# Optimization experiments

Measured on AMD Instinct MI355X. Metric: run time of the kernel, lower is better.

The kernel has to match this reference:

```python
import jax, jax.numpy as jnp
import numpy as np

ACT_MIN, ACT_MAX = -127.0, 127.0      # 8-bit symmetric
W_MIN, W_MAX = -127.0, 127.0          # 8-bit symmetric
B_MIN, B_MAX = -32767.0, 32767.0      # 16-bit symmetric
ALPHA = 10.0                          # clipped-ReLU ceiling


def fake_quant(x, min_v, max_v):
    # 'scale' quantization: per-tensor symmetric scale from max-abs,
    # round -> clamp -> dequant; straight-through estimator for grads.
    scale = max_v / jnp.max(jnp.abs(x))
    q = jnp.clip(jnp.round(x * scale), min_v, max_v) / scale
    return x + jax.lax.stop_gradient(q - x)


def qconv(x, w, b, stride, pad):
    wq = fake_quant(w, W_MIN, W_MAX)
    bq = fake_quant(b, B_MIN, B_MAX)
    y = jax.lax.conv_general_dilated(
        x, wq, (stride, stride), [(pad, pad), (pad, pad)],
        dimension_numbers=('NCHW', 'OIHW', 'NCHW'))
    return y + bq[None, :, None, None]


def qrelu(x):
    return fake_quant(jnp.clip(x, 0.0, ALPHA), ACT_MIN, ACT_MAX)


def maxpool(x, k, s, p):
    return jax.lax.reduce_window(
        x, -jnp.inf, jax.lax.max,
        (1, 1, k, k), (1, 1, s, s),
        [(0, 0), (0, 0), (p, p), (p, p)])


def setup_inputs() -> dict:
    key = jax.random.key(0)
    ks = jax.random.split(key, 13)

    def kaiming(k, shape):
        fan_in = int(np.prod(shape[1:]))
        return jax.random.normal(k, shape, jnp.float32) * np.sqrt(2.0 / fan_in)

    return {
        'x':  jax.random.normal(ks[0], (4096, 1, 32, 32), jnp.float32),
        'w1': kaiming(ks[1], (32, 1, 3, 3)),  'b1': jnp.zeros((32,), jnp.float32) + 0.01,
        'w2': kaiming(ks[2], (64, 32, 3, 3)), 'b2': jnp.zeros((64,), jnp.float32) + 0.01,
        'w3': kaiming(ks[3], (16, 64, 1, 1)), 'b3': jnp.zeros((16,), jnp.float32) + 0.01,
        'w4': kaiming(ks[4], (16, 16, 3, 3)), 'b4': jnp.zeros((16,), jnp.float32) + 0.01,
        'w5': kaiming(ks[5], (64, 16, 1, 1)), 'b5': jnp.zeros((64,), jnp.float32) + 0.01,
        'wl': kaiming(ks[6], (10, 64)),       'bl': jnp.zeros((10,), jnp.float32) + 0.01,
    }


def reference(x, w1, b1, w2, b2, w3, b3, w4, b4, w5, b5, wl, bl):
    x = fake_quant(x, ACT_MIN, ACT_MAX)           # quantize input acts
    x_skip1 = maxpool(x, 5, 4, 2)                 # [B,1,8,8]
    out = qrelu(qconv(x, w1, b1, 2, 1))           # [B,32,16,16]
    out = qconv(out, w2, b2, 2, 1)                # [B,64,8,8]
    out = qrelu(out + x_skip1)                    # broadcast 1ch skip over 64ch
    x_skip2 = maxpool(out, 3, 2, 1)               # [B,64,4,4]
    out = qrelu(qconv(out, w3, b3, 1, 0))         # [B,16,8,8]
    out = qrelu(qconv(out, w4, b4, 2, 1))         # [B,16,4,4]
    out = qconv(out, w5, b5, 1, 0)                # [B,64,4,4]
    out = qrelu(out + x_skip2)
    out = jnp.mean(out, axis=(2, 3))              # avgpool 4x4 -> [B,64]
    wq = fake_quant(wl, W_MIN, W_MAX)
    bq = fake_quant(bl, B_MIN, B_MAX)
    return out @ wq.T + bq                        # [B,10]
```

## Files before the change

kernel.cpp:

```cpp
#include <hip/hip_runtime.h>

#define BATCH 4096

typedef __attribute__((ext_vector_type(8))) short bf16x8;
typedef __attribute__((ext_vector_type(4))) float f32x4;

constexpr int OFF_MAXARR = 1024;
constexpr int OFF_W1Q = 8192;
constexpr int OFF_W2Q = OFF_W1Q + 288;
constexpr int OFF_W3Q = OFF_W2Q + 18432;
constexpr int OFF_W4Q = OFF_W3Q + 1024;
constexpr int OFF_W5Q = OFF_W4Q + 2304;
constexpr int OFF_WLQ = OFF_W5Q + 1024;
constexpr int OFF_B1Q = OFF_WLQ + 640;
constexpr int OFF_B2Q = OFF_B1Q + 32;
constexpr int OFF_B3Q = OFF_B2Q + 64;
constexpr int OFF_B4Q = OFF_B3Q + 16;
constexpr int OFF_B5Q = OFF_B4Q + 16;
constexpr int OFF_BLQ = OFF_B5Q + 64;
constexpr int OFF_W1I = 32768;
constexpr int OFF_W2I = OFF_W1I + 512;
constexpr int OFF_W3I = OFF_W2I + 9216;
constexpr size_t OFF_SK1F = 49152;
constexpr size_t OFF_V2   = OFF_SK1F + (size_t)BATCH * 64;
constexpr size_t OFF_SK2I = OFF_V2 + (size_t)BATCH * 4096;
constexpr size_t OFF_A3   = OFF_SK2I + (size_t)BATCH * 512;
constexpr size_t OFF_A4   = OFF_A3 + (size_t)BATCH * 1024;
constexpr size_t OFF_A5   = OFF_A4 + (size_t)BATCH * 256;
constexpr size_t WS_FLOATS_NEEDED = OFF_A5 + (size_t)BATCH * 1024;

#define A1_S   40
#define A1_ROW (18 * A1_S)

__device__ __forceinline__ float fq(float x, float scale, float maxv) {
    float q = rintf(x * scale);
    q = fminf(fmaxf(q, -maxv), maxv);
    return q / scale;
}

__device__ __forceinline__ short int_to_bf16_bits(float v) {
    return (short)(__float_as_uint(v) >> 16);
}

__device__ __forceinline__ float bf16_bits_to_float(short b) {
    return __uint_as_float(((unsigned)(unsigned short)b) << 16);
}

__device__ __forceinline__ void block_max_spread(float v, unsigned* arr, float* red4) {
#pragma unroll
    for (int off = 32; off; off >>= 1) v = fmaxf(v, __shfl_xor(v, off, 64));
    int tid = threadIdx.x;
    if ((tid & 63) == 0) red4[tid >> 6] = v;
    __syncthreads();
    if (tid == 0) {
        float m = fmaxf(fmaxf(red4[0], red4[1]), fmaxf(red4[2], red4[3]));
        atomicMax(&arr[(blockIdx.x & 63) << 4], __float_as_uint(m));
    }
    __syncthreads();
}

__device__ __forceinline__ float load_spread_max(const unsigned* arr, float* bc) {
    int tid = threadIdx.x;
    if (tid < 64) {
        float v = __uint_as_float(arr[tid << 4]);
#pragma unroll
        for (int off = 32; off; off >>= 1) v = fmaxf(v, __shfl_xor(v, off, 64));
        if (tid == 0) *bc = v;
    }
    __syncthreads();
    return *bc;
}

__device__ __forceinline__ void stage_xq(const float* xi, float sx, short* xt_q, int tid) {
    for (int i = tid; i < 1024; i += 256) {
        int ih = i >> 5, iw = i & 31;
        float q = rintf(xi[i] * sx);
        q = fminf(fmaxf(q, -127.f), 127.f);
        xt_q[(ih + 1) * 34 + (iw + 1)] = int_to_bf16_bits(q);
    }
}

__device__ __forceinline__ bf16x8 load_a1frag(const short* xt_q, int pos, int kslot) {
    bf16x8 a = {0, 0, 0, 0, 0, 0, 0, 0};
    int oh = pos >> 4, ow = pos & 15;
    const short* base = xt_q + (oh * 2) * 34 + ow * 2;
    if (kslot == 0) {
        a[0] = base[0];  a[1] = base[1];  a[2] = base[2];
        a[3] = base[34]; a[4] = base[35]; a[5] = base[36];
        a[6] = base[68]; a[7] = base[69];
    } else if (kslot == 1) {
        a[0] = base[70];
    }
    return a;
}

struct PrepArgs {
    const float* src[12];
    float*       dst[12];
    int          n[12];
    float        maxv[12];
    const float* w1; short* w1i; float* inv1;
    const float* w2; short* w2i; float* inv2;
    const float* w3; short* w3i; float* inv3;
    const float4* x; int n4; unsigned* xarr;
};

__global__ __launch_bounds__(256) void k_prep(PrepArgs P) {
    __shared__ float red[256];
    __shared__ float red4[4];
    int b = blockIdx.x, tid = threadIdx.x;
    if (b < 12) {
        const float* s = P.src[b];
        float* d = P.dst[b];
        int n = P.n[b];
        float maxv = P.maxv[b];
        float m = 0.f;
        for (int i = tid; i < n; i += 256) m = fmaxf(m, fabsf(s[i]));
        red[tid] = m;
        __syncthreads();
        for (int sft = 128; sft > 0; sft >>= 1) {
            if (tid < sft) red[tid] = fmaxf(red[tid], red[tid + sft]);
            __syncthreads();
        }
        float scale = maxv / red[0];
        for (int i = tid; i < n; i += 256) {
            float q = rintf(s[i] * scale);
            q = fminf(fmaxf(q, -maxv), maxv);
            d[i] = q / scale;
        }
    } else if (b == 12) {
        float m = 0.f;
        for (int i = tid; i < 288; i += 256) m = fmaxf(m, fabsf(P.w1[i]));
        red[tid] = m;
        __syncthreads();
        for (int s = 128; s > 0; s >>= 1) {
            if (tid < s) red[tid] = fmaxf(red[tid], red[tid + s]);
            __syncthreads();
        }
        float maxw = red[0];
        float sw = 127.f / maxw;
        if (tid == 0) *P.inv1 = maxw / 127.f;
        for (int i = tid; i < 1024; i += 256) P.w1i[i] = 0;
        __syncthreads();
        for (int i = tid; i < 288; i += 256) {
            int oc = i / 9, t = i % 9;
            float q = rintf(P.w1[i] * sw);
            q = fminf(fmaxf(q, -127.f), 127.f);
            P.w1i[oc * 32 + t] = int_to_bf16_bits(q);
        }
    } else if (b == 13) {
        float m = 0.f;
        for (int i = tid; i < 18432; i += 256) m = fmaxf(m, fabsf(P.w2[i]));
        red[tid] = m;
        __syncthreads();
        for (int s = 128; s > 0; s >>= 1) {
            if (tid < s) red[tid] = fmaxf(red[tid], red[tid + s]);
            __syncthreads();
        }
        float maxw = red[0];
        float sw = 127.f / maxw;
        if (tid == 0) *P.inv2 = maxw / 127.f;
        for (int i = tid; i < 18432; i += 256) {
            int oc = i / 288, r = i % 288, ic = r / 9, t = r % 9;
            float q = rintf(P.w2[i] * sw);
            q = fminf(fmaxf(q, -127.f), 127.f);
            P.w2i[oc * 288 + t * 32 + ic] = int_to_bf16_bits(q);
        }
    } else if (b == 14) {
        float m = 0.f;
        for (int i = tid; i < 1024; i += 256) m = fmaxf(m, fabsf(P.w3[i]));
        red[tid] = m;
        __syncthreads();
        for (int s = 128; s > 0; s >>= 1) {
            if (tid < s) red[tid] = fmaxf(red[tid], red[tid + s]);
            __syncthreads();
        }
        float maxw = red[0];
        float sw = 127.f / maxw;
        if (tid == 0) *P.inv3 = maxw / 127.f;
        for (int i = tid; i < 1024; i += 256) {
            float q = rintf(P.w3[i] * sw);
            q = fminf(fmaxf(q, -127.f), 127.f);
            P.w3i[i] = int_to_bf16_bits(q);
        }
    } else {
        float m = 0.f;
        int nb = gridDim.x - 15;
        for (int i = (b - 15) * 256 + tid; i < P.n4; i += nb * 256) {
            float4 v = P.x[i];
            m = fmaxf(m, fmaxf(fmaxf(fabsf(v.x), fabsf(v.y)), fmaxf(fabsf(v.z), fabsf(v.w))));
        }
        block_max_spread(m, P.xarr, red4);
    }
}

__global__ __launch_bounds__(256) void k_s1(const float* __restrict__ x,
                                            const short* __restrict__ w1i,
                                            const float* __restrict__ b1q,
                                            const unsigned* xmaxarr,
                                            const float* __restrict__ inv_sw1p,
                                            float* __restrict__ skip1f,
                                            unsigned* m1arr) {
    __shared__ short xt_q[34 * 34];
    __shared__ float red4[4];
    __shared__ float bc0;
    int tid = threadIdx.x, lane = tid & 63, wv = tid >> 6;
    int kslot = lane >> 4;
    float xmax = load_spread_max(xmaxarr, &bc0);
    float sx = 127.f / xmax;
    float inv1 = (*inv_sw1p) / sx;
    bf16x8 w1b[2];
#pragma unroll
    for (int nb = 0; nb < 2; nb++)
        w1b[nb] = *(const bf16x8*)(w1i + (nb * 16 + (lane & 15)) * 32 + kslot * 8);
    float bias1[2] = {b1q[lane & 15], b1q[16 + (lane & 15)]};

    for (int i = tid; i < 34 * 34; i += 256) xt_q[i] = 0;

    float lmax = 0.f;
    for (int li = 0; li < 4; li++) {
        int img = blockIdx.x * 4 + li;
        __syncthreads();
        stage_xq(x + (size_t)img * 1024, sx, xt_q, tid);
        __syncthreads();
        if (tid < 64) {
            int soh = tid >> 3, sow = tid & 7;
            float m = -INFINITY;
            int h0 = soh * 4 - 2, w0 = sow * 4 - 2;
            for (int kh = 0; kh < 5; kh++) {
                int ih = h0 + kh;
                if (ih < 0 || ih >= 32) continue;
                for (int kw = 0; kw < 5; kw++) {
                    int iw = w0 + kw;
                    if (iw < 0 || iw >= 32) continue;
                    m = fmaxf(m, bf16_bits_to_float(xt_q[(ih + 1) * 34 + (iw + 1)]));
                }
            }
            skip1f[img * 64 + tid] = m / sx;
        }
        f32x4 acc[4][2] = {};
#pragma unroll
        for (int mb = 0; mb < 4; mb++) {
            bf16x8 a = load_a1frag(xt_q, (wv * 4 + mb) * 16 + (lane & 15), kslot);
#pragma unroll
            for (int nb = 0; nb < 2; nb++)
                acc[mb][nb] = __builtin_amdgcn_mfma_f32_16x16x32_bf16(a, w1b[nb], acc[mb][nb], 0, 0, 0);
        }
#pragma unroll
        for (int mb = 0; mb < 4; mb++)
#pragma unroll
            for (int nb = 0; nb < 2; nb++)
#pragma unroll
                for (int r = 0; r < 4; r++) {
                    float v = acc[mb][nb][r] * inv1 + bias1[nb];
                    lmax = fmaxf(lmax, fminf(fmaxf(v, 0.f), 10.f));
                }
    }
    block_max_spread(lmax, m1arr, red4);
}

__global__ __launch_bounds__(256) void k_s2(const float* __restrict__ x,
                                            const short* __restrict__ w1i,
                                            const float* __restrict__ b1q,
                                            const short* __restrict__ w2i,
                                            const float* __restrict__ b2q,
                                            const float* __restrict__ skip1f,
                                            const unsigned* xmaxarr, const unsigned* m1arr,
                                            const float* __restrict__ inv_sw1p,
                                            const float* __restrict__ inv_sw2p,
                                            float* __restrict__ v2w,
                                            unsigned* m2arr) {
    __shared__ short xt_q[34 * 34];
    __shared__ short a1t[18 * A1_ROW];
    __shared__ float sk1s[64];
    __shared__ float red4[4];
    __shared__ float bc0, bc1;
    int tid = threadIdx.x, lane = tid & 63, wv = tid >> 6;
    int kslot = lane >> 4;
    float xmax = load_spread_max(xmaxarr, &bc0);
    float m1 = load_spread_max(m1arr, &bc1);
    float sx = 127.f / xmax;
    float inv1 = (*inv_sw1p) / sx;
    float s1q = 127.f / m1;
    float inv2 = (m1 / 127.f) * (*inv_sw2p);

    bf16x8 w1b[2];
#pragma unroll
    for (int nb = 0; nb < 2; nb++)
        w1b[nb] = *(const bf16x8*)(w1i + (nb * 16 + (lane & 15)) * 32 + kslot * 8);
    float bias1[2] = {b1q[lane & 15], b1q[16 + (lane & 15)]};
    int oc2 = wv * 16 + (lane & 15);
    bf16x8 bw2[9];
#pragma unroll
    for (int t = 0; t < 9; t++)
        bw2[t] = *(const bf16x8*)(w2i + oc2 * 288 + t * 32 + kslot * 8);
    float bias2 = b2q[oc2];

    for (int i = tid; i < 34 * 34; i += 256) xt_q[i] = 0;
    for (int i = tid; i < 18 * A1_ROW / 2; i += 256) ((int*)a1t)[i] = 0;

    float lmax = 0.f;
    for (int li = 0; li < 4; li++) {
        int img = blockIdx.x * 4 + li;
        __syncthreads();
        stage_xq(x + (size_t)img * 1024, sx, xt_q, tid);
        if (tid < 64) sk1s[tid] = skip1f[img * 64 + tid];
        __syncthreads();
        f32x4 acc1[4][2] = {};
#pragma unroll
        for (int mb = 0; mb < 4; mb++) {
            bf16x8 a = load_a1frag(xt_q, (wv * 4 + mb) * 16 + (lane & 15), kslot);
#pragma unroll
            for (int nb = 0; nb < 2; nb++)
                acc1[mb][nb] = __builtin_amdgcn_mfma_f32_16x16x32_bf16(a, w1b[nb], acc1[mb][nb], 0, 0, 0);
        }
#pragma unroll
        for (int mb = 0; mb < 4; mb++)
#pragma unroll
            for (int nb = 0; nb < 2; nb++)
#pragma unroll
                for (int r = 0; r < 4; r++) {
                    float v = acc1[mb][nb][r] * inv1 + bias1[nb];
                    v = fminf(fmaxf(v, 0.f), 10.f);
                    float q = fminf(rintf(v * s1q), 127.f);
                    int pos = (wv * 4 + mb) * 16 + (lane >> 4) * 4 + r;
                    int oc = nb * 16 + (lane & 15);
                    a1t[((pos >> 4) + 1) * A1_ROW + ((pos & 15) + 1) * A1_S + oc] =
                        int_to_bf16_bits(q);
                }
        __syncthreads();
        float* vo = v2w + (size_t)img * 4096;
#pragma unroll
        for (int mb = 0; mb < 4; mb++) {
            int m = mb * 16 + (lane & 15);
            int oh = m >> 3, ow = m & 7;
            const short* abase = a1t + (oh * 2) * A1_ROW + (ow * 2) * A1_S + kslot * 8;
            f32x4 acc = {0.f, 0.f, 0.f, 0.f};
#pragma unroll
            for (int kh = 0; kh < 3; kh++)
#pragma unroll
                for (int kw = 0; kw < 3; kw++) {
                    bf16x8 av = *(const bf16x8*)(abase + kh * A1_ROW + kw * A1_S);
                    acc = __builtin_amdgcn_mfma_f32_16x16x32_bf16(av, bw2[kh * 3 + kw], acc, 0, 0, 0);
                }
            float4 vv;
            float* vvp = (float*)&vv;
#pragma unroll
            for (int r = 0; r < 4; r++) {
                int pos = mb * 16 + (lane >> 4) * 4 + r;
                float v = acc[r] * inv2 + bias2 + sk1s[pos];
                v = fminf(fmaxf(v, 0.f), 10.f);
                vvp[r] = v;
                lmax = fmaxf(lmax, v);
            }
            *(float4*)(vo + oc2 * 64 + mb * 16 + (lane >> 4) * 4) = vv;
        }
    }
    block_max_spread(lmax, m2arr, red4);
}

__global__ __launch_bounds__(256) void k_s3(const float* __restrict__ v2w,
                                            const short* __restrict__ w3i,
                                            const float* __restrict__ b3q,
                                            const unsigned* m2arr,
                                            const float* __restrict__ inv_sw3p,
                                            float* __restrict__ a3w,
                                            short* __restrict__ sk2q,
                                            unsigned* m3arr) {
    __shared__ short a2q[64 * 64];
    __shared__ float red4[4];
    __shared__ float bc0;
    int tid = threadIdx.x, lane = tid & 63, wv = tid >> 6;
    float m2 = load_spread_max(m2arr, &bc0);
    float s2 = 127.f / m2;
    float inv3 = (m2 / 127.f) * (*inv_sw3p);
    int oc2 = wv * 16 + (lane & 15);
    bf16x8 bw3[2];
#pragma unroll
    for (int t = 0; t < 2; t++)
        bw3[t] = *(const bf16x8*)(w3i + (lane & 15) * 64 + t * 32 + (lane >> 4) * 8);
    float bias3 = b3q[lane & 15];

    float lmax = 0.f;
    for (int li = 0; li < 4; li++) {
        int img = blockIdx.x * 4 + li;
        __syncthreads();
        const float* vi = v2w + (size_t)img * 4096;
#pragma unroll
        for (int mb = 0; mb < 4; mb++) {
            float4 vv = *(const float4*)(vi + oc2 * 64 + mb * 16 + (lane >> 4) * 4);
            const float* vvp = (const float*)&vv;
#pragma unroll
            for (int r = 0; r < 4; r++) {
                int pos = mb * 16 + (lane >> 4) * 4 + r;
                float q = fminf(rintf(vvp[r] * s2), 127.f);
                a2q[pos * 64 + oc2] = int_to_bf16_bits(q);
            }
        }
        __syncthreads();
        const short* abase = a2q + (wv * 16 + (lane & 15)) * 64 + (lane >> 4) * 8;
        f32x4 acc = {0.f, 0.f, 0.f, 0.f};
#pragma unroll
        for (int t = 0; t < 2; t++) {
            bf16x8 av = *(const bf16x8*)(abase + t * 32);
            acc = __builtin_amdgcn_mfma_f32_16x16x32_bf16(av, bw3[t], acc, 0, 0, 0);
        }
        float* a3o = a3w + (size_t)img * 1024;
#pragma unroll
        for (int r = 0; r < 4; r++) {
            int pos = wv * 16 + (lane >> 4) * 4 + r;
            float v = acc[r] * inv3 + bias3;
            v = fminf(fmaxf(v, 0.f), 10.f);
            a3o[(lane & 15) * 64 + pos] = v;
            lmax = fmaxf(lmax, v);
        }
        short* sko = sk2q + (size_t)img * 1024;
#pragma unroll
        for (int r = 0; r < 4; ++r) {
            int idx = tid * 4 + r;
            int c = idx >> 4, pp = idx & 15, soh = pp >> 2, sow = pp & 3;
            float m = -INFINITY;
            for (int kh = 0; kh < 3; kh++) {
                int ih = soh * 2 - 1 + kh;
                if (ih < 0 || ih >= 8) continue;
                for (int kw = 0; kw < 3; kw++) {
                    int iw = sow * 2 - 1 + kw;
                    if (iw < 0 || iw >= 8) continue;
                    m = fmaxf(m, bf16_bits_to_float(a2q[(ih * 8 + iw) * 64 + c]));
                }
            }
            sko[idx] = int_to_bf16_bits(m);
        }
    }
    block_max_spread(lmax, m3arr, red4);
}

__global__ __launch_bounds__(256) void k_conv4(const float* __restrict__ a3,
                                               const float* __restrict__ w4q,
                                               const float* __restrict__ b4q,
                                               const unsigned* m3arr,
                                               float* __restrict__ a4,
                                               unsigned* m4arr) {
    __shared__ float tile[16 * 10 * 10];
    __shared__ float red4[4];
    __shared__ float bc0;
    int b = blockIdx.x, tid = threadIdx.x;
    float m3 = load_spread_max(m3arr, &bc0);
    float s3 = 127.f / m3;
    for (int i = tid; i < 1600; i += 256) tile[i] = 0.f;
    __syncthreads();
    const float* ai = a3 + (size_t)b * 1024;
    for (int i = tid; i < 1024; i += 256) {
        int ic = i >> 6, p = i & 63, ih = p >> 3, iw = p & 7;
        float q = rintf(ai[i] * s3);
        q = fminf(fmaxf(q, -127.f), 127.f);
        tile[ic * 100 + (ih + 1) * 10 + (iw + 1)] = q / s3;
    }
    __syncthreads();
    int oc = tid >> 4, p = tid & 15, oh = p >> 2, ow = p & 3;
    float acc = b4q[oc];
    const float* w = w4q + oc * 144;
    for (int ic = 0; ic < 16; ic++) {
        const float* tin = tile + ic * 100 + (oh * 2) * 10 + (ow * 2);
        const float* wc = w + ic * 9;
#pragma unroll
        for (int kh = 0; kh < 3; kh++)
#pragma unroll
            for (int kw = 0; kw < 3; kw++)
                acc += tin[kh * 10 + kw] * wc[kh * 3 + kw];
    }
    float v = fminf(fmaxf(acc, 0.f), 10.f);
    a4[(size_t)b * 256 + tid] = v;
    block_max_spread(v, m4arr, red4);
}

__global__ __launch_bounds__(256) void k_conv5(const float* __restrict__ a4,
                                               const float* __restrict__ w5q,
                                               const float* __restrict__ b5q,
                                               const short* __restrict__ sk2q,
                                               const unsigned* m2arr,
                                               const unsigned* m4arr,
                                               float* __restrict__ a5,
                                               unsigned* m5arr) {
    __shared__ float tin[256];
    __shared__ float red4[4];
    __shared__ float bc0, bc1;
    int b = blockIdx.x, tid = threadIdx.x;
    float m2 = load_spread_max(m2arr, &bc0);
    float m4 = load_spread_max(m4arr, &bc1);
    float s4 = 127.f / m4;
    float invs2 = m2 / 127.f;
    const float* ai = a4 + (size_t)b * 256;
    {
        float q = rintf(ai[tid] * s4);
        q = fminf(fmaxf(q, -127.f), 127.f);
        tin[tid] = q / s4;
    }
    __syncthreads();
    int p = tid & 15, ocb = tid >> 4;
    float lmax = 0.f;
    float* o = a5 + (size_t)b * 1024;
    for (int j = 0; j < 4; j++) {
        int oc = ocb * 4 + j;
        float acc = b5q[oc];
        const float* w = w5q + oc * 16;
#pragma unroll
        for (int ic = 0; ic < 16; ic++) acc += tin[ic * 16 + p] * w[ic];
        acc += bf16_bits_to_float(sk2q[(size_t)b * 1024 + oc * 16 + p]) * invs2;
        float v = fminf(fmaxf(acc, 0.f), 10.f);
        o[oc * 16 + p] = v;
        lmax = fmaxf(lmax, v);
    }
    block_max_spread(lmax, m5arr, red4);
}

__global__ __launch_bounds__(64) void k_head(const float* __restrict__ a5,
                                             const unsigned* m5arr,
                                             const float* __restrict__ wlq,
                                             const float* __restrict__ blq,
                                             float* __restrict__ out) {
    __shared__ float h[64];
    __shared__ float bc0;
    int b = blockIdx.x, c = threadIdx.x;
    float m5 = load_spread_max(m5arr, &bc0);
    float s5 = 127.f / m5;
    const float* ai = a5 + (size_t)b * 1024 + c * 16;
    float sum = 0.f;
#pragma unroll
    for (int p = 0; p < 16; p++) sum += fq(ai[p], s5, 127.f);
    h[c] = sum * (1.f / 16.f);
    __syncthreads();
    if (c < 10) {
        float acc = blq[c];
        const float* w = wlq + c * 64;
        for (int ic = 0; ic < 64; ic++) acc = fmaf(h[ic], w[ic], acc);
        out[(size_t)b * 10 + c] = acc;
    }
}

extern "C" void kernel_launch(void* const* d_in, const int* in_sizes, int n_in,
                              void* d_out, int out_size, void* d_ws, size_t ws_size,
                              hipStream_t stream) {
    const float* x  = (const float*)d_in[0];
    const float* w1 = (const float*)d_in[1];
    const float* b1 = (const float*)d_in[2];
    const float* w2 = (const float*)d_in[3];
    const float* b2 = (const float*)d_in[4];
    const float* w3 = (const float*)d_in[5];
    const float* b3 = (const float*)d_in[6];
    const float* w4 = (const float*)d_in[7];
    const float* b4 = (const float*)d_in[8];
    const float* w5 = (const float*)d_in[9];
    const float* b5 = (const float*)d_in[10];
    const float* wl = (const float*)d_in[11];
    const float* bl = (const float*)d_in[12];

    if (ws_size < WS_FLOATS_NEEDED * sizeof(float)) return;

    float* ws = (float*)d_ws;
    unsigned* slots = (unsigned*)d_ws;
    unsigned* marr[6];
    for (int k = 0; k < 6; k++) marr[k] = slots + OFF_MAXARR + k * 1024;
    short* w1i = (short*)(ws + OFF_W1I);
    short* w2i = (short*)(ws + OFF_W2I);
    short* w3i = (short*)(ws + OFF_W3I);

    hipMemsetAsync(d_ws, 0, 32768, stream);

    PrepArgs P;
    const float* srcs[12] = {w1, w2, w3, w4, w5, wl, b1, b2, b3, b4, b5, bl};
    const int    ns[12]   = {288, 18432, 1024, 2304, 1024, 640, 32, 64, 16, 16, 64, 10};
    const int    offs[12] = {OFF_W1Q, OFF_W2Q, OFF_W3Q, OFF_W4Q, OFF_W5Q, OFF_WLQ,
                             OFF_B1Q, OFF_B2Q, OFF_B3Q, OFF_B4Q, OFF_B5Q, OFF_BLQ};
    const float  mv[12]   = {127.f, 127.f, 127.f, 127.f, 127.f, 127.f,
                             32767.f, 32767.f, 32767.f, 32767.f, 32767.f, 32767.f};
    for (int i = 0; i < 12; i++) {
        P.src[i] = srcs[i];
        P.dst[i] = ws + offs[i];
        P.n[i] = ns[i];
        P.maxv[i] = mv[i];
    }
    P.w1 = w1; P.w1i = w1i; P.inv1 = ws + 8;
    P.w2 = w2; P.w2i = w2i; P.inv2 = ws + 6;
    P.w3 = w3; P.w3i = w3i; P.inv3 = ws + 7;
    P.x = (const float4*)x; P.n4 = BATCH * 256; P.xarr = marr[0];

    k_prep<<<15 + 256, 256, 0, stream>>>(P);
    k_s1<<<BATCH / 4, 256, 0, stream>>>(x, w1i, ws + OFF_B1Q, marr[0], ws + 8,
                                        ws + OFF_SK1F, marr[1]);
    k_s2<<<BATCH / 4, 256, 0, stream>>>(x, w1i, ws + OFF_B1Q, w2i, ws + OFF_B2Q,
                                        ws + OFF_SK1F, marr[0], marr[1], ws + 8, ws + 6,
                                        ws + OFF_V2, marr[2]);
    k_s3<<<BATCH / 4, 256, 0, stream>>>(ws + OFF_V2, w3i, ws + OFF_B3Q, marr[2], ws + 7,
                                        ws + OFF_A3, (short*)(ws + OFF_SK2I), marr[3]);
    k_conv4<<<BATCH, 256, 0, stream>>>(ws + OFF_A3, ws + OFF_W4Q, ws + OFF_B4Q, marr[3],
                                       ws + OFF_A4, marr[4]);
    k_conv5<<<BATCH, 256, 0, stream>>>(ws + OFF_A4, ws + OFF_W5Q, ws + OFF_B5Q,
                                       (const short*)(ws + OFF_SK2I), marr[2], marr[4],
                                       ws + OFF_A5, marr[5]);
    k_head<<<BATCH, 64, 0, stream>>>(ws + OFF_A5, marr[5], ws + OFF_WLQ, ws + OFF_BLQ,
                                     (float*)d_out);
}
```

Before: 210.6 us.

## Store conv1 output as uint8 and recompute conv2 in stage 3

Stage 2 no longer writes the fp32 conv2 output (16 KB per image). Instead it stores the quantized conv1 activations as uint8 (8 KB per image) and only computes conv2 to get the global max. Stage 3 reloads those bytes, rebuilds the padded bf16 tile in LDS and recomputes conv2 with MFMA before quantizing and running conv3. The skip2 tensor is also stored as uint8 instead of bf16. This trades duplicated conv2 MFMA work and an extra LDS buffer for a large cut in global memory traffic.

```diff
diff --git a/kernel.cpp b/kernel.cpp
--- a/kernel.cpp
+++ b/kernel.cpp
@@ -22,9 +22,9 @@
 constexpr int OFF_W2I = OFF_W1I + 512;
 constexpr int OFF_W3I = OFF_W2I + 9216;
 constexpr size_t OFF_SK1F = 49152;
-constexpr size_t OFF_V2   = OFF_SK1F + (size_t)BATCH * 64;
-constexpr size_t OFF_SK2I = OFF_V2 + (size_t)BATCH * 4096;
-constexpr size_t OFF_A3   = OFF_SK2I + (size_t)BATCH * 512;
+constexpr size_t OFF_A1Q  = OFF_SK1F + (size_t)BATCH * 64;
+constexpr size_t OFF_SK2U = OFF_A1Q + (size_t)BATCH * 2048;
+constexpr size_t OFF_A3   = OFF_SK2U + (size_t)BATCH * 256;
 constexpr size_t OFF_A4   = OFF_A3 + (size_t)BATCH * 1024;
 constexpr size_t OFF_A5   = OFF_A4 + (size_t)BATCH * 256;
 constexpr size_t WS_FLOATS_NEEDED = OFF_A5 + (size_t)BATCH * 1024;
@@ -268,10 +268,11 @@
                                             const unsigned* xmaxarr, const unsigned* m1arr,
                                             const float* __restrict__ inv_sw1p,
                                             const float* __restrict__ inv_sw2p,
-                                            float* __restrict__ v2w,
+                                            unsigned char* __restrict__ a1qw,
                                             unsigned* m2arr) {
     __shared__ short xt_q[34 * 34];
     __shared__ short a1t[18 * A1_ROW];
+    __shared__ unsigned char u8buf[256 * 32];
     __shared__ float sk1s[64];
     __shared__ float red4[4];
     __shared__ float bc0, bc1;
@@ -327,9 +328,15 @@
                     int oc = nb * 16 + (lane & 15);
                     a1t[((pos >> 4) + 1) * A1_ROW + ((pos & 15) + 1) * A1_S + oc] =
                         int_to_bf16_bits(q);
+                    u8buf[pos * 32 + oc] = (unsigned char)q;
                 }
         __syncthreads();
-        float* vo = v2w + (size_t)img * 4096;
+        {
+            uint4* dst = (uint4*)(a1qw + (size_t)img * 8192);
+            const uint4* src = (const uint4*)u8buf;
+            dst[tid * 2] = src[tid * 2];
+            dst[tid * 2 + 1] = src[tid * 2 + 1];
+        }
 #pragma unroll
         for (int mb = 0; mb < 4; mb++) {
             int m = mb * 16 + (lane & 15);
@@ -343,62 +350,97 @@
                     bf16x8 av = *(const bf16x8*)(abase + kh * A1_ROW + kw * A1_S);
                     acc = __builtin_amdgcn_mfma_f32_16x16x32_bf16(av, bw2[kh * 3 + kw], acc, 0, 0, 0);
                 }
-            float4 vv;
-            float* vvp = (float*)&vv;
 #pragma unroll
             for (int r = 0; r < 4; r++) {
                 int pos = mb * 16 + (lane >> 4) * 4 + r;
                 float v = acc[r] * inv2 + bias2 + sk1s[pos];
                 v = fminf(fmaxf(v, 0.f), 10.f);
-                vvp[r] = v;
                 lmax = fmaxf(lmax, v);
             }
-            *(float4*)(vo + oc2 * 64 + mb * 16 + (lane >> 4) * 4) = vv;
         }
     }
     block_max_spread(lmax, m2arr, red4);
 }
 
-__global__ __launch_bounds__(256) void k_s3(const float* __restrict__ v2w,
+__global__ __launch_bounds__(256) void k_s3(const unsigned char* __restrict__ a1qw,
+                                            const short* __restrict__ w2i,
+                                            const float* __restrict__ b2q,
+                                            const float* __restrict__ skip1f,
                                             const short* __restrict__ w3i,
                                             const float* __restrict__ b3q,
-                                            const unsigned* m2arr,
+                                            const unsigned* m1arr, const unsigned* m2arr,
+                                            const float* __restrict__ inv_sw2p,
                                             const float* __restrict__ inv_sw3p,
                                             float* __restrict__ a3w,
-                                            short* __restrict__ sk2q,
+                                            unsigned char* __restrict__ sk2u,
                                             unsigned* m3arr) {
+    __shared__ short a1t[18 * A1_ROW];
     __shared__ short a2q[64 * 64];
+    __shared__ float sk1s[64];
     __shared__ float red4[4];
-    __shared__ float bc0;
+    __shared__ float bc0, bc1;
     int tid = threadIdx.x, lane = tid & 63, wv = tid >> 6;
-    float m2 = load_spread_max(m2arr, &bc0);
+    int kslot = lane >> 4;
+    float m1 = load_spread_max(m1arr, &bc0);
+    float m2 = load_spread_max(m2arr, &bc1);
+    float inv2 = (m1 / 127.f) * (*inv_sw2p);
     float s2 = 127.f / m2;
     float inv3 = (m2 / 127.f) * (*inv_sw3p);
     int oc2 = wv * 16 + (lane & 15);
+    bf16x8 bw2[9];
+#pragma unroll
+    for (int t = 0; t < 9; t++)
+        bw2[t] = *(const bf16x8*)(w2i + oc2 * 288 + t * 32 + kslot * 8);
+    float bias2 = b2q[oc2];
     bf16x8 bw3[2];
 #pragma unroll
     for (int t = 0; t < 2; t++)
-        bw3[t] = *(const bf16x8*)(w3i + (lane & 15) * 64 + t * 32 + (lane >> 4) * 8);
+        bw3[t] = *(const bf16x8*)(w3i + (lane & 15) * 64 + t * 32 + kslot * 8);
     float bias3 = b3q[lane & 15];
+
+    for (int i = tid; i < 18 * A1_ROW / 2; i += 256) ((int*)a1t)[i] = 0;
 
     float lmax = 0.f;
     for (int li = 0; li < 4; li++) {
         int img = blockIdx.x * 4 + li;
         __syncthreads();
-        const float* vi = v2w + (size_t)img * 4096;
+        {
+            uint4 u0 = ((const uint4*)(a1qw + (size_t)img * 8192))[tid * 2];
+            uint4 u1 = ((const uint4*)(a1qw + (size_t)img * 8192))[tid * 2 + 1];
+            const unsigned char* qb = (const unsigned char*)&u0;
+            short* dst = a1t + ((tid >> 4) + 1) * A1_ROW + ((tid & 15) + 1) * A1_S;
+#pragma unroll
+            for (int c = 0; c < 16; c++) dst[c] = int_to_bf16_bits((float)qb[c]);
+            qb = (const unsigned char*)&u1;
+#pragma unroll
+            for (int c = 0; c < 16; c++) dst[16 + c] = int_to_bf16_bits((float)qb[c]);
+        }
+        if (tid < 64) sk1s[tid] = skip1f[img * 64 + tid];
+        __syncthreads();
 #pragma unroll
         for (int mb = 0; mb < 4; mb++) {
-            float4 vv = *(const float4*)(vi + oc2 * 64 + mb * 16 + (lane >> 4) * 4);
-            const float* vvp = (const float*)&vv;
+            int m = mb * 16 + (lane & 15);
+            int oh = m >> 3, ow = m & 7;
+            const short* abase = a1t + (oh * 2) * A1_ROW + (ow * 2) * A1_S + kslot * 8;
+            f32x4 acc = {0.f, 0.f, 0.f, 0.f};
+#pragma unroll
+            for (int kh = 0; kh < 3; kh++)
+#pragma unroll
+                for (int kw = 0; kw < 3; kw++) {
+                    bf16x8 av = *(const bf16x8*)(abase + kh * A1_ROW + kw * A1_S);
+                    acc = __builtin_amdgcn_mfma_f32_16x16x32_bf16(av, bw2[kh * 3 + kw], acc, 0, 0, 0);
+                }
 #pragma unroll
             for (int r = 0; r < 4; r++) {
                 int pos = mb * 16 + (lane >> 4) * 4 + r;
-                float q = fminf(rintf(vvp[r] * s2), 127.f);
+                float v = acc[r] * inv2 + bias2 + sk1s[pos];
+                v = fminf(fmaxf(v, 0.f), 10.f);
+                float q = fminf(rintf(v * s2), 127.f);
                 a2q[pos * 64 + oc2] = int_to_bf16_bits(q);
             }
         }
         __syncthreads();
-        const short* abase = a2q + (wv * 16 + (lane & 15)) * 64 + (lane >> 4) * 8;
+        const short* abase = a2q + (wv * 16 + (lane & 15)) * 64 + kslot * 8;
         f32x4 acc = {0.f, 0.f, 0.f, 0.f};
 #pragma unroll
         for (int t = 0; t < 2; t++) {
@@ -414,7 +456,7 @@
             a3o[(lane & 15) * 64 + pos] = v;
             lmax = fmaxf(lmax, v);
         }
-        short* sko = sk2q + (size_t)img * 1024;
+        unsigned char* sko = sk2u + (size_t)img * 1024;
 #pragma unroll
         for (int r = 0; r < 4; ++r) {
             int idx = tid * 4 + r;
@@ -429,7 +471,7 @@
                     m = fmaxf(m, bf16_bits_to_float(a2q[(ih * 8 + iw) * 64 + c]));
                 }
             }
-            sko[idx] = int_to_bf16_bits(m);
+            sko[idx] = (unsigned char)m;
         }
     }
     block_max_spread(lmax, m3arr, red4);
@@ -477,7 +519,7 @@
 __global__ __launch_bounds__(256) void k_conv5(const float* __restrict__ a4,
                                                const float* __restrict__ w5q,
                                                const float* __restrict__ b5q,
-                                               const short* __restrict__ sk2q,
+                                               const unsigned char* __restrict__ sk2u,
                                                const unsigned* m2arr,
                                                const unsigned* m4arr,
                                                float* __restrict__ a5,
@@ -506,7 +548,7 @@
         const float* w = w5q + oc * 16;
 #pragma unroll
         for (int ic = 0; ic < 16; ic++) acc += tin[ic * 16 + p] * w[ic];
-        acc += bf16_bits_to_float(sk2q[(size_t)b * 1024 + oc * 16 + p]) * invs2;
+        acc += (float)sk2u[(size_t)b * 1024 + oc * 16 + p] * invs2;
         float v = fminf(fmaxf(acc, 0.f), 10.f);
         o[oc * 16 + p] = v;
         lmax = fmaxf(lmax, v);
@@ -564,6 +606,8 @@
     short* w1i = (short*)(ws + OFF_W1I);
     short* w2i = (short*)(ws + OFF_W2I);
     short* w3i = (short*)(ws + OFF_W3I);
+    unsigned char* a1q = (unsigned char*)(ws + OFF_A1Q);
+    unsigned char* sk2u = (unsigned char*)(ws + OFF_SK2U);
 
     hipMemsetAsync(d_ws, 0, 32768, stream);
 
@@ -590,13 +634,14 @@
                                         ws + OFF_SK1F, marr[1]);
     k_s2<<<BATCH / 4, 256, 0, stream>>>(x, w1i, ws + OFF_B1Q, w2i, ws + OFF_B2Q,
                                         ws + OFF_SK1F, marr[0], marr[1], ws + 8, ws + 6,
-                                        ws + OFF_V2, marr[2]);
-    k_s3<<<BATCH / 4, 256, 0, stream>>>(ws + OFF_V2, w3i, ws + OFF_B3Q, marr[2], ws + 7,
-                                        ws + OFF_A3, (short*)(ws + OFF_SK2I), marr[3]);
+                                        a1q, marr[2]);
+    k_s3<<<BATCH / 4, 256, 0, stream>>>(a1q, w2i, ws + OFF_B2Q, ws + OFF_SK1F,
+                                        w3i, ws + OFF_B3Q, marr[1], marr[2], ws + 6, ws + 7,
+                                        ws + OFF_A3, sk2u, marr[3]);
     k_conv4<<<BATCH, 256, 0, stream>>>(ws + OFF_A3, ws + OFF_W4Q, ws + OFF_B4Q, marr[3],
                                        ws + OFF_A4, marr[4]);
     k_conv5<<<BATCH, 256, 0, stream>>>(ws + OFF_A4, ws + OFF_W5Q, ws + OFF_B5Q,
-                                       (const short*)(ws + OFF_SK2I), marr[2], marr[4],
+                                       sk2u, marr[2], marr[4],
                                        ws + OFF_A5, marr[5]);
     k_head<<<BATCH, 64, 0, stream>>>(ws + OFF_A5, marr[5], ws + OFF_WLQ, ws + OFF_BLQ,
                                      (float*)d_out);
```

Result: slower. 227.4 us (+8.0%).
